# Kernel tuning notes

Measured on AMD Instinct MI355X. Metric: run time of the kernel, lower is better.

The kernel has to match this reference:

```python
import jax, jax.numpy as jnp
import numpy as np

B, V, H, L = 2, 256, 128, 3
GROUPS = 32  # GroupNorm32 in the 'normalization' head
EPS = 1e-5


def _layernorm(z, g, b):
    m = jnp.mean(z, -1, keepdims=True)
    v = jnp.var(z, -1, keepdims=True)
    return (z - m) * jax.lax.rsqrt(v + EPS) * g + b


def _forward(x, adj_matrix, emb_type, W_node, b_node, W_eattr, b_eattr, W_ee, b_ee,
             Wu, bu, Wv, bv, Wa, ba, Wb, bb, Wc, bc,
             lnh_g, lnh_b, lne_g, lne_b, plo_g, plo_b, plo_W, plo_bW,
             gn_g, gn_b, W_out, b_out):
    # node embed: Embedding(2,H) lookup -> Linear(H,H)
    h = emb_type[x] @ W_node + b_node                      # B V H
    ea = jnp.transpose(adj_matrix, (0, 2, 3, 1))           # B V V 6
    # edge embed: Linear(6,H) -> Linear(H,H)
    e = (ea @ W_eattr + b_eattr) @ W_ee + b_ee             # B V V H
    # graph = graph[..., -6].long(): binary adjacency channel, no grad
    mask = jax.lax.stop_gradient(ea[..., 0])               # B V V
    for l in range(L):
        h_in, e_in = h, e
        # gated anisotropic GCN layer (DIFUSCO GNNLayer, mode='direct')
        Uh = h @ Wu[l] + bu[l]                             # B V H
        Vh = h @ Wv[l] + bv[l]                             # B V H
        e_new = ((h @ Wa[l] + ba[l])[:, None, :, :]
                 + (h @ Wb[l] + bb[l])[:, :, None, :]
                 + (e @ Wc[l] + bc[l]))                    # B V V H
        gates = jax.nn.sigmoid(e_new) * mask[..., None]    # B V V H
        agg = jnp.einsum('bijh,bjh->bih', gates, Vh)       # gated 'sum' aggregation
        h = jax.nn.relu(_layernorm(Uh + agg, lnh_g[l], lnh_b[l]))
        e = jax.nn.relu(_layernorm(e_new, lne_g[l], lne_b[l]))
        # outer residual (GNNDi.dense_forward) + per_layer_out: LN -> SiLU -> Linear
        h = h_in + h
        e = e_in + (jax.nn.silu(_layernorm(e, plo_g[l], plo_b[l])) @ plo_W[l] + plo_bW[l])
    # head: GroupNorm(32,H) -> ReLU -> Conv2d(H, out_channels, 1) on B H V V
    z = jnp.transpose(e, (0, 3, 1, 2))                     # B H V V
    zg = z.reshape(B, GROUPS, H // GROUPS, V, V)
    mu = jnp.mean(zg, axis=(2, 3, 4), keepdims=True)
    var = jnp.var(zg, axis=(2, 3, 4), keepdims=True)
    z = ((zg - mu) * jax.lax.rsqrt(var + EPS)).reshape(B, H, V, V)
    z = jax.nn.relu(z * gn_g[None, :, None, None] + gn_b[None, :, None, None])
    return jnp.einsum('bchw,oc->bohw', z, W_out) + b_out[None, :, None, None]


def setup_inputs() -> dict:
    key = jax.random.key(0)
    ks = jax.random.split(key, 16)
    nrm = lambda k, s: jax.random.normal(k, s, dtype=jnp.float32) * 0.05
    adj = jnp.concatenate([
        (jax.random.uniform(ks[1], (B, 1, V, V)) < 0.15).astype(jnp.float32),  # channel 0: adjacency
        jax.random.normal(ks[2], (B, 5, V, V), dtype=jnp.float32)], axis=1)
    return {
        'x': jax.random.randint(ks[0], (B, V), 0, 2),
        'adj_matrix': adj,
        'emb_type': nrm(ks[3], (2, H)),
        'W_node': nrm(ks[4], (H, H)), 'b_node': jnp.zeros((H,), jnp.float32),
        'W_eattr': nrm(ks[5], (6, H)), 'b_eattr': jnp.zeros((H,), jnp.float32),
        'W_ee': nrm(ks[6], (H, H)), 'b_ee': jnp.zeros((H,), jnp.float32),
        'Wu': nrm(ks[7], (L, H, H)), 'bu': jnp.zeros((L, H), jnp.float32),
        'Wv': nrm(ks[8], (L, H, H)), 'bv': jnp.zeros((L, H), jnp.float32),
        'Wa': nrm(ks[9], (L, H, H)), 'ba': jnp.zeros((L, H), jnp.float32),
        'Wb': nrm(ks[10], (L, H, H)), 'bb': jnp.zeros((L, H), jnp.float32),
        'Wc': nrm(ks[11], (L, H, H)), 'bc': jnp.zeros((L, H), jnp.float32),
        'lnh_g': jnp.ones((L, H), jnp.float32), 'lnh_b': jnp.zeros((L, H), jnp.float32),
        'lne_g': jnp.ones((L, H), jnp.float32), 'lne_b': jnp.zeros((L, H), jnp.float32),
        'plo_g': jnp.ones((L, H), jnp.float32), 'plo_b': jnp.zeros((L, H), jnp.float32),
        'plo_W': nrm(ks[12], (L, H, H)), 'plo_bW': jnp.zeros((L, H), jnp.float32),
        'gn_g': jnp.ones((H,), jnp.float32), 'gn_b': jnp.zeros((H,), jnp.float32),
        'W_out': nrm(ks[13], (1, H)), 'b_out': jnp.zeros((1,), jnp.float32),
    }


def reference(x, adj_matrix, emb_type, W_node, b_node, W_eattr, b_eattr, W_ee, b_ee,
              Wu, bu, Wv, bv, Wa, ba, Wb, bb, Wc, bc,
              lnh_g, lnh_b, lne_g, lne_b, plo_g, plo_b, plo_W, plo_bW,
              gn_g, gn_b, W_out, b_out):
    return _forward(x, adj_matrix, emb_type, W_node, b_node, W_eattr, b_eattr, W_ee, b_ee,
                    Wu, bu, Wv, bv, Wa, ba, Wb, bb, Wc, bc,
                    lnh_g, lnh_b, lne_g, lne_b, plo_g, plo_b, plo_W, plo_bW,
                    gn_g, gn_b, W_out, b_out)
```

## Files before the change

### kernel.cpp

```cpp
#include <hip/hip_runtime.h>
#include <cstdint>
#include <cstddef>


#define EPSV 1e-5f

typedef __attribute__((ext_vector_type(8))) short short8v;
typedef __attribute__((ext_vector_type(4))) float f32x4;

__device__ __forceinline__ float sigmoidf_(float x) { return 1.f / (1.f + __expf(-x)); }

__device__ __forceinline__ unsigned short f2bf(float x) {
    unsigned int u = __float_as_uint(x);
    unsigned int r = u + 0x7FFFu + ((u >> 16) & 1u);
    return (unsigned short)(r >> 16);
}
__device__ __forceinline__ float bf2f(unsigned short u) {
    return __uint_as_float(((unsigned int)u) << 16);
}
__device__ __forceinline__ unsigned int cvtpk(float a, float b) {
    unsigned int r;
    asm("v_cvt_pk_bf16_f32 %0, %1, %2" : "=v"(r) : "v"(a), "v"(b));
    return r;
}
#define SWZ(row, cb) ((cb) ^ (((row) & 7) << 4))

__global__ void k_prep(const int* __restrict__ x, const float* __restrict__ emb,
                       const float* __restrict__ W_node, const float* __restrict__ b_node,
                       float* __restrict__ h, float* __restrict__ aggB,
                       const float* __restrict__ W_ea, const float* __restrict__ b_ea,
                       const float* __restrict__ W_ee, const float* __restrict__ b_ee,
                       float* __restrict__ Wcb, float* __restrict__ bcb,
                       const float* __restrict__ Wc, const float* __restrict__ PW,
                       unsigned short* __restrict__ WT)
{
    const int blk = blockIdx.x, t = threadIdx.x;
    if (blk < 512) {
        __shared__ float se[128];
        if (t < 128) { se[t] = emb[x[blk]*128 + t]; aggB[blk*128 + t] = 0.f; }
        __syncthreads();
        if (t < 128) {
            float acc = b_node[t];
            for (int k = 0; k < 128; ++k) acc = fmaf(se[k], W_node[k*128+t], acc);
            h[blk*128+t] = acc;
        }
    } else if (blk == 512) {
        if (t < 128) {
            float wc0=0,wc1=0,wc2=0,wc3=0,wc4=0,wc5=0,bv=0;
            for (int m = 0; m < 128; ++m) {
                float we = W_ee[m*128 + t];
                wc0 = fmaf(W_ea[0*128+m], we, wc0);
                wc1 = fmaf(W_ea[1*128+m], we, wc1);
                wc2 = fmaf(W_ea[2*128+m], we, wc2);
                wc3 = fmaf(W_ea[3*128+m], we, wc3);
                wc4 = fmaf(W_ea[4*128+m], we, wc4);
                wc5 = fmaf(W_ea[5*128+m], we, wc5);
                bv  = fmaf(b_ea[m], we, bv);
            }
            Wcb[0*128+t]=wc0; Wcb[1*128+t]=wc1; Wcb[2*128+t]=wc2;
            Wcb[3*128+t]=wc3; Wcb[4*128+t]=wc4; Wcb[5*128+t]=wc5;
            bcb[t] = bv + b_ee[t];
        }
    } else {
        const int m = blk - 513;
        const int l = m >> 1;
        const float* src = (m & 1) ? (PW + (size_t)l*16384) : (Wc + (size_t)l*16384);
        unsigned short* dst = WT + (size_t)m*16384;
        for (int idx = t; idx < 16384; idx += 256) {
            int n = idx >> 7, k = idx & 127;
            dst[idx] = f2bf(src[k*128 + n]);
        }
    }
}

__global__ void k_hgemm(float* __restrict__ h, float* __restrict__ Uh, float* __restrict__ aggB,
    const float* __restrict__ Wu_l, const float* __restrict__ bu_l,
    const float* __restrict__ Wv_l, const float* __restrict__ bv_l,
    const float* __restrict__ Wa_l, const float* __restrict__ ba_l,
    const float* __restrict__ Wb_l, const float* __restrict__ bb_l,
    float* __restrict__ VhT, float* __restrict__ AhT, float* __restrict__ Bh,
    const float* __restrict__ lnh_g, const float* __restrict__ lnh_b, int upd)
{
    __shared__ float sh[128];
    __shared__ float sred[4];
    int blk = blockIdx.x, t = threadIdx.x;
    int b = blk >> 8, v = blk & 255;
    float hv_ = h[blk*128 + t];
    if (upd) {
        float val = Uh[blk*128 + t] + aggB[blk*128 + t];
        aggB[blk*128 + t] = 0.f;
        float s = val, q = val*val;
        #pragma unroll
        for (int off = 32; off; off >>= 1) { s += __shfl_down(s, off); q += __shfl_down(q, off); }
        if ((t & 63) == 0) { sred[t>>6] = s; sred[2 + (t>>6)] = q; }
        __syncthreads();
        s = sred[0] + sred[1]; q = sred[2] + sred[3];
        float mean = s * (1.f/128.f);
        float var  = q * (1.f/128.f) - mean*mean;
        float nv = (val - mean) * rsqrtf(var + EPSV) * lnh_g[t] + lnh_b[t];
        hv_ += fmaxf(nv, 0.f);
        h[blk*128 + t] = hv_;
    }
    sh[t] = hv_;
    __syncthreads();
    float au=bu_l[t], av=bv_l[t], aa=ba_l[t], ab=bb_l[t];
    for (int k = 0; k < 128; ++k) {
        float hv = sh[k];
        au = fmaf(hv, Wu_l[k*128+t], au);
        av = fmaf(hv, Wv_l[k*128+t], av);
        aa = fmaf(hv, Wa_l[k*128+t], aa);
        ab = fmaf(hv, Wb_l[k*128+t], ab);
    }
    Uh[blk*128+t]=au; Bh[blk*128+t]=ab;
    VhT[(size_t)(b*128+t)*256 + v] = av;
    AhT[(size_t)(b*128+t)*256 + v] = aa;
}

template<int EINIT, int DO_AGG, int DO_STATS>
__global__ __launch_bounds__(256) void k_layer(
    unsigned short* __restrict__ e,
    const unsigned short* __restrict__ WcT, const unsigned short* __restrict__ PWT,
    const float* __restrict__ bc_l,
    const float* __restrict__ AhT, const float* __restrict__ Bh,
    const float* __restrict__ VhT, const float* __restrict__ adj,
    const float* __restrict__ lne_g, const float* __restrict__ lne_b,
    const float* __restrict__ plo_g, const float* __restrict__ plo_b,
    const float* __restrict__ pbW_l,
    float* __restrict__ aggB,
    const float* __restrict__ Wcb, const float* __restrict__ bcb,
    float* __restrict__ ggsum, float* __restrict__ ggsq)
{
    __shared__ __align__(16) char sW[32768];
    __shared__ float sRedA[512];
    __shared__ float sRedB[512];

    const int t = threadIdx.x;
    const int bi = blockIdx.x >> 2, chunk = blockIdx.x & 3;
    const int b = bi >> 8, i = bi & 255;
    const int w = t >> 6, lane = t & 63;
    const int lane16 = lane & 15, g = lane >> 4;
    const size_t rowbase = (size_t)bi * 32768;
    const int j0 = chunk*64 + w*16;
    char* sE = sW + w*4096;

    short8v a8[4];
    float am[6];
    if (EINIT) {
        const float* adjp = adj + (size_t)b*393216 + (size_t)i*256 + (j0 + lane16);
        #pragma unroll
        for (int m = 0; m < 6; ++m) am[m] = adjp[(size_t)m*65536];
        #pragma unroll
        for (int kst = 0; kst < 4; ++kst) {
            short8v v;
            #pragma unroll
            for (int e2 = 0; e2 < 4; ++e2) {
                const int h0 = kst*32 + g*8 + e2*2;
                float v0 = bcb[h0], v1 = bcb[h0+1];
                #pragma unroll
                for (int m = 0; m < 6; ++m) {
                    v0 = fmaf(am[m], Wcb[m*128 + h0],     v0);
                    v1 = fmaf(am[m], Wcb[m*128 + h0 + 1], v1);
                }
                const unsigned int p = cvtpk(v0, v1);
                v[e2*2]   = (short)(unsigned short)p;
                v[e2*2+1] = (short)(unsigned short)(p >> 16);
            }
            a8[kst] = v;
        }
    } else {
        const unsigned short* arow = e + rowbase + (size_t)(j0 + lane16)*128 + g*8;
        #pragma unroll
        for (int kst = 0; kst < 4; ++kst)
            a8[kst] = *(const short8v*)&arow[kst*32];
    }

    #pragma unroll
    for (int p = 0; p < 8; ++p) {
        const int idx = t*8 + p*2048;
        const int n = idx >> 7, cb = (idx & 127) << 1;
        *(short8v*)(sW + n*256 + SWZ(n, cb)) = *(const short8v*)&WcT[idx];
    }
    __syncthreads();

    f32x4 tv[8];
    float agg[8];
    float s1[4] = {0,0,0,0}, q1[4] = {0,0,0,0};
    const int jb = j0 + g*4;
    float4 mk;
    if (DO_AGG) mk = *(const float4*)&adj[(size_t)b*393216 + (size_t)i*256 + jb];
    const float* mkp = (const float*)&mk;
    #pragma unroll
    for (int nt = 0; nt < 8; ++nt) {
        const int col = nt*16 + lane16;
        f32x4 acc = {0.f,0.f,0.f,0.f};
        #pragma unroll
        for (int kst = 0; kst < 4; ++kst) {
            short8v bfr = *(const short8v*)(sW + col*256 + SWZ(col, kst*64 + g*16));
            acc = __builtin_amdgcn_mfma_f32_16x16x32_bf16(a8[kst], bfr, acc, 0, 0, 0);
        }
        const float bcB = bc_l[col] + Bh[bi*128 + col];
        const float4 ah = *(const float4*)&AhT[(size_t)(b*128+col)*256 + jb];
        const float* ahp = (const float*)&ah;
        if (DO_AGG) {
            const float4 vh = *(const float4*)&VhT[(size_t)(b*128+col)*256 + jb];
            const float* vhp = (const float*)&vh;
            float a = 0.f;
            #pragma unroll
            for (int r = 0; r < 4; ++r) {
                float tvl = acc[r] + bcB + ahp[r];
                a = fmaf(mkp[r]*sigmoidf_(tvl), vhp[r], a);
                s1[r] += tvl; q1[r] = fmaf(tvl, tvl, q1[r]);
                tv[nt][r] = tvl;
            }
            agg[nt] = a;
        } else {
            #pragma unroll
            for (int r = 0; r < 4; ++r) {
                float tvl = acc[r] + bcB + ahp[r];
                s1[r] += tvl; q1[r] = fmaf(tvl, tvl, q1[r]);
                tv[nt][r] = tvl;
            }
        }
    }
    float mu1[4], rs1[4];
    #pragma unroll
    for (int r = 0; r < 4; ++r) {
        float s = s1[r], q = q1[r];
        s += __shfl_xor(s,1); q += __shfl_xor(q,1);
        s += __shfl_xor(s,2); q += __shfl_xor(q,2);
        s += __shfl_xor(s,4); q += __shfl_xor(q,4);
        s += __shfl_xor(s,8); q += __shfl_xor(q,8);
        float mu = s*(1.f/128.f);
        mu1[r] = mu; rs1[r] = rsqrtf(q*(1.f/128.f) - mu*mu + EPSV);
    }
    float s2[4] = {0,0,0,0}, q2[4] = {0,0,0,0};
    #pragma unroll
    for (int nt = 0; nt < 8; ++nt) {
        const int col = nt*16 + lane16;
        const float lg = lne_g[col], lb = lne_b[col];
        #pragma unroll
        for (int r = 0; r < 4; ++r) {
            float tp = fmaxf(fmaf((tv[nt][r]-mu1[r])*rs1[r], lg, lb), 0.f);
            tv[nt][r] = tp;
            s2[r] += tp; q2[r] = fmaf(tp, tp, q2[r]);
        }
    }
    float mu2[4], rs2[4];
    #pragma unroll
    for (int r = 0; r < 4; ++r) {
        float s = s2[r], q = q2[r];
        s += __shfl_xor(s,1); q += __shfl_xor(q,1);
        s += __shfl_xor(s,2); q += __shfl_xor(q,2);
        s += __shfl_xor(s,4); q += __shfl_xor(q,4);
        s += __shfl_xor(s,8); q += __shfl_xor(q,8);
        float mu = s*(1.f/128.f);
        mu2[r] = mu; rs2[r] = rsqrtf(q*(1.f/128.f) - mu*mu + EPSV);
    }

    __syncthreads();

    #pragma unroll
    for (int nt = 0; nt < 8; ++nt) {
        const int col = nt*16 + lane16;
        const float pg = plo_g[col], pb = plo_b[col];
        float u[4];
        #pragma unroll
        for (int r = 0; r < 4; ++r) {
            float uu = fmaf((tv[nt][r]-mu2[r])*rs2[r], pg, pb);
            u[r] = uu * sigmoidf_(uu);
        }
        const unsigned int p01 = cvtpk(u[0], u[1]);
        const unsigned int p23 = cvtpk(u[2], u[3]);
        const int r0 = g*4;
        *(unsigned short*)(sE + (r0+0)*256 + SWZ(r0+0, col*2)) = (unsigned short)p01;
        *(unsigned short*)(sE + (r0+1)*256 + SWZ(r0+1, col*2)) = (unsigned short)(p01 >> 16);
        *(unsigned short*)(sE + (r0+2)*256 + SWZ(r0+2, col*2)) = (unsigned short)p23;
        *(unsigned short*)(sE + (r0+3)*256 + SWZ(r0+3, col*2)) = (unsigned short)(p23 >> 16);
    }
    short8v b8[4];
    #pragma unroll
    for (int kst = 0; kst < 4; ++kst)
        b8[kst] = *(const short8v*)(sE + lane16*256 + SWZ(lane16, kst*64 + g*16));

    __syncthreads();
    #pragma unroll
    for (int p = 0; p < 8; ++p) {
        const int idx = t*8 + p*2048;
        const int n = idx >> 7, cb = (idx & 127) << 1;
        *(short8v*)(sW + n*256 + SWZ(n, cb)) = *(const short8v*)&PWT[idx];
    }
    __syncthreads();

    const int jg = j0 + lane16;
    float gs[8], gq[8];
    #pragma unroll
    for (int nt = 0; nt < 8; ++nt) {
        const int an = nt*16 + lane16;
        f32x4 acc = {0.f,0.f,0.f,0.f};
        #pragma unroll
        for (int kst = 0; kst < 4; ++kst) {
            short8v aw = *(const short8v*)(sW + an*256 + SWZ(an, kst*64 + g*16));
            acc = __builtin_amdgcn_mfma_f32_16x16x32_bf16(aw, b8[kst], acc, 0, 0, 0);
        }
        const int n0 = nt*16 + g*4;
        const float4 pw4 = *(const float4*)&pbW_l[n0];
        const float* pwp = (const float*)&pw4;
        unsigned short* ep = &e[rowbase + (size_t)jg*128 + n0];
        float res[4];
        if (EINIT) {
            #pragma unroll
            for (int r = 0; r < 4; ++r) {
                float v0 = bcb[n0 + r];
                #pragma unroll
                for (int m = 0; m < 6; ++m) v0 = fmaf(am[m], Wcb[m*128 + n0 + r], v0);
                res[r] = v0;
            }
        } else {
            const ushort4 ev = *(const ushort4*)ep;
            res[0] = bf2f(ev.x); res[1] = bf2f(ev.y); res[2] = bf2f(ev.z); res[3] = bf2f(ev.w);
        }
        const float o0 = acc[0] + (pwp[0] + res[0]);
        const float o1 = acc[1] + (pwp[1] + res[1]);
        const float o2 = acc[2] + (pwp[2] + res[2]);
        const float o3 = acc[3] + (pwp[3] + res[3]);
        if (DO_STATS) {
            gs[nt] = (o0 + o1) + (o2 + o3);
            gq[nt] = fmaf(o0,o0, fmaf(o1,o1, fmaf(o2,o2, o3*o3)));
        }
        uint2 st;
        st.x = cvtpk(o0, o1);
        st.y = cvtpk(o2, o3);
        *(uint2*)ep = st;
    }

    if (DO_AGG) {
        #pragma unroll
        for (int nt = 0; nt < 8; ++nt) {
            float a = agg[nt];
            a += __shfl_xor(a, 16); a += __shfl_xor(a, 32);
            if (lane < 16) sRedA[w*128 + nt*16 + lane] = a;
        }
        __syncthreads();
        if (t < 128) {
            float S = sRedA[t] + sRedA[128+t] + sRedA[256+t] + sRedA[384+t];
            atomicAdd(&aggB[bi*128 + t], S);
        }
    }
    if (DO_STATS) {
        #pragma unroll
        for (int nt = 0; nt < 8; ++nt) {
            float a = gs[nt], qq = gq[nt];
            a += __shfl_xor(a, 1); qq += __shfl_xor(qq, 1);
            a += __shfl_xor(a, 2); qq += __shfl_xor(qq, 2);
            a += __shfl_xor(a, 4); qq += __shfl_xor(qq, 4);
            a += __shfl_xor(a, 8); qq += __shfl_xor(qq, 8);
            if (lane16 == 0) {
                sRedA[w*32 + nt*4 + g] = a;
                sRedB[w*32 + nt*4 + g] = qq;
            }
        }
        __syncthreads();
        if (t < 32) {
            float S = sRedA[t] + sRedA[32+t] + sRedA[64+t] + sRedA[96+t];
            float Q = sRedB[t] + sRedB[32+t] + sRedB[64+t] + sRedB[96+t];
            atomicAdd(&ggsum[b*32 + t], S);
            atomicAdd(&ggsq[b*32 + t], Q);
        }
    }
}

__global__ void k_gfin(const float* __restrict__ ggsum, const float* __restrict__ ggsq,
                       float* __restrict__ gmu, float* __restrict__ grs)
{
    int t = threadIdx.x;
    float s = ggsum[t], q = ggsq[t];
    const float invN = 1.f/(4.f*65536.f);
    float mu = s*invN;
    float var = q*invN - mu*mu;
    gmu[t] = mu;
    grs[t] = rsqrtf(var + EPSV);
}

__global__ __launch_bounds__(256) void k_head(
    const unsigned short* __restrict__ e, const float* __restrict__ gmu,
    const float* __restrict__ grs, const float* __restrict__ gn_g,
    const float* __restrict__ gn_b, const float* __restrict__ W_out,
    const float* __restrict__ b_out, float* __restrict__ out)
{
    const int blk = blockIdx.x, t = threadIdx.x;
    const int b = blk >> 8;
    const int ch8 = (t & 15)*8, jgrp = t >> 4;
    float gg[8], gb[8], wo[8];
    #pragma unroll
    for (int c = 0; c < 8; ++c) {
        const int ch = ch8 + c;
        const float mu = gmu[b*32 + (ch>>2)], rs = grs[b*32 + (ch>>2)];
        gg[c] = gn_g[ch]*rs;
        gb[c] = gn_b[ch] - mu*gg[c];
        wo[c] = W_out[ch];
    }
    const float bo = b_out[0];
    const unsigned short* erow = e + (size_t)blk*32768;
    float* orow = out + (size_t)blk*256;
    for (int it = 0; it < 16; ++it) {
        const int j = jgrp*16 + it;
        short8v v = *(const short8v*)&erow[(size_t)j*128 + ch8];
        float p = 0.f;
        #pragma unroll
        for (int c = 0; c < 8; ++c) {
            float f = bf2f((unsigned short)v[c]);
            p = fmaf(fmaxf(fmaf(f, gg[c], gb[c]), 0.f), wo[c], p);
        }
        p += __shfl_xor(p, 1); p += __shfl_xor(p, 2);
        p += __shfl_xor(p, 4); p += __shfl_xor(p, 8);
        if ((t & 15) == 0) orow[j] = p + bo;
    }
}

extern "C" void kernel_launch(void* const* d_in, const int* in_sizes, int n_in,
                              void* d_out, int out_size, void* d_ws, size_t ws_size,
                              hipStream_t stream)
{
    const int*   x      = (const int*)  d_in[0];
    const float* adj    = (const float*)d_in[1];
    const float* emb    = (const float*)d_in[2];
    const float* W_node = (const float*)d_in[3];
    const float* b_node = (const float*)d_in[4];
    const float* W_ea   = (const float*)d_in[5];
    const float* b_ea   = (const float*)d_in[6];
    const float* W_ee   = (const float*)d_in[7];
    const float* b_ee   = (const float*)d_in[8];
    const float* Wu     = (const float*)d_in[9];
    const float* bu     = (const float*)d_in[10];
    const float* Wv     = (const float*)d_in[11];
    const float* bv     = (const float*)d_in[12];
    const float* Wa     = (const float*)d_in[13];
    const float* ba     = (const float*)d_in[14];
    const float* Wb     = (const float*)d_in[15];
    const float* bb     = (const float*)d_in[16];
    const float* Wc     = (const float*)d_in[17];
    const float* bc     = (const float*)d_in[18];
    const float* lnh_g  = (const float*)d_in[19];
    const float* lnh_b  = (const float*)d_in[20];
    const float* lne_g  = (const float*)d_in[21];
    const float* lne_b  = (const float*)d_in[22];
    const float* plo_g  = (const float*)d_in[23];
    const float* plo_b  = (const float*)d_in[24];
    const float* plo_W  = (const float*)d_in[25];
    const float* plo_bW = (const float*)d_in[26];
    const float* gn_g   = (const float*)d_in[27];
    const float* gn_b   = (const float*)d_in[28];
    const float* W_out  = (const float*)d_in[29];
    const float* b_out  = (const float*)d_in[30];
    float* out = (float*)d_out;

    float* ws = (float*)d_ws;
    size_t off = 0;
    unsigned short* e = (unsigned short*)(ws + off); off += 8388608;
    float* h    = ws + off; off += 65536;
    float* Uh   = ws + off; off += 65536;
    float* Bh   = ws + off; off += 65536;
    float* VhT  = ws + off; off += 65536;
    float* AhT  = ws + off; off += 65536;
    float* aggB = ws + off; off += 65536;
    float* Wcb  = ws + off; off += 768;
    float* bcb  = ws + off; off += 128;
    float* ggsum = ws + off; off += 64;
    float* ggsq  = ws + off; off += 64;
    float* gmu  = ws + off; off += 64;
    float* grs  = ws + off; off += 64;
    unsigned short* WT = (unsigned short*)(ws + off); off += 49152;

    k_prep<<<519, 256, 0, stream>>>(x, emb, W_node, b_node, h, aggB,
                                    W_ea, b_ea, W_ee, b_ee, Wcb, bcb,
                                    Wc, plo_W, WT);
    hipMemsetAsync(ggsum, 0, 512, stream);

    for (int l = 0; l < 3; ++l) {
        k_hgemm<<<512, 128, 0, stream>>>(h, Uh, aggB,
            Wu + (size_t)l*16384, bu + l*128,
            Wv + (size_t)l*16384, bv + l*128,
            Wa + (size_t)l*16384, ba + l*128,
            Wb + (size_t)l*16384, bb + l*128,
            VhT, AhT, Bh,
            lnh_g + (l==0?0:(l-1)*128), lnh_b + (l==0?0:(l-1)*128), l > 0 ? 1 : 0);
        const unsigned short* WcT_l = WT + (size_t)(2*l)*16384;
        const unsigned short* PWT_l = WT + (size_t)(2*l+1)*16384;
        if (l == 0) {
            k_layer<1,1,0><<<2048, 256, 0, stream>>>(e, WcT_l, PWT_l,
                bc + l*128, AhT, Bh, VhT, adj,
                lne_g + l*128, lne_b + l*128,
                plo_g + l*128, plo_b + l*128,
                plo_bW + l*128, aggB, Wcb, bcb, ggsum, ggsq);
        } else if (l == 1) {
            k_layer<0,1,0><<<2048, 256, 0, stream>>>(e, WcT_l, PWT_l,
                bc + l*128, AhT, Bh, VhT, adj,
                lne_g + l*128, lne_b + l*128,
                plo_g + l*128, plo_b + l*128,
                plo_bW + l*128, aggB, Wcb, bcb, ggsum, ggsq);
        } else {
            k_layer<0,0,1><<<2048, 256, 0, stream>>>(e, WcT_l, PWT_l,
                bc + l*128, AhT, Bh, VhT, adj,
                lne_g + l*128, lne_b + l*128,
                plo_g + l*128, plo_b + l*128,
                plo_bW + l*128, aggB, Wcb, bcb, ggsum, ggsq);
        }
    }

    k_gfin<<<1, 64, 0, stream>>>(ggsum, ggsq, gmu, grs);
    k_head<<<512, 256, 0, stream>>>(e, gmu, grs, gn_g, gn_b, W_out, b_out, out);
}
```

Before: 234.5 us.

## Double-buffer Wc and plo_W in LDS, use 512-thread blocks per half-row

The per-layer edge kernel now uses 512-thread blocks, each covering half of an edge row instead of a quarter. Both weight matrices (Wc and the per-layer-out weight) are loaded into separate LDS buffers up front, which removes the mid-kernel barrier pair and the weight reload between the two GEMMs. The first layer now writes the initial edge embedding to global memory during init and reads it back as the residual, instead of recomputing it from the adjacency. This halves weight staging per edge, at the cost of more LDS per block (about 69 KB) and so fewer resident blocks.

New measurement: 250.3 us. 6.7% more time.

```diff
diff --git a/kernel.cpp b/kernel.cpp
--- a/kernel.cpp
+++ b/kernel.cpp
@@ -117,7 +117,7 @@
 }
 
 template<int EINIT, int DO_AGG, int DO_STATS>
-__global__ __launch_bounds__(256) void k_layer(
+__global__ __launch_bounds__(512, 4) void k_layer(
     unsigned short* __restrict__ e,
     const unsigned short* __restrict__ WcT, const unsigned short* __restrict__ PWT,
     const float* __restrict__ bc_l,
@@ -130,42 +130,51 @@
     const float* __restrict__ Wcb, const float* __restrict__ bcb,
     float* __restrict__ ggsum, float* __restrict__ ggsq)
 {
-    __shared__ __align__(16) char sW[32768];
-    __shared__ float sRedA[512];
-    __shared__ float sRedB[512];
+    __shared__ __align__(16) char sW1[32768];
+    __shared__ __align__(16) char sW2[32768];
+    __shared__ float sRedA[1024];
+    __shared__ float sRedB[256];
 
     const int t = threadIdx.x;
-    const int bi = blockIdx.x >> 2, chunk = blockIdx.x & 3;
+    const int bi = blockIdx.x >> 1, half = blockIdx.x & 1;
     const int b = bi >> 8, i = bi & 255;
     const int w = t >> 6, lane = t & 63;
     const int lane16 = lane & 15, g = lane >> 4;
     const size_t rowbase = (size_t)bi * 32768;
-    const int j0 = chunk*64 + w*16;
-    char* sE = sW + w*4096;
+    const int j0 = half*128 + w*16;
+    char* sE = sW1 + w*4096;
 
     short8v a8[4];
-    float am[6];
     if (EINIT) {
+        float am[6];
         const float* adjp = adj + (size_t)b*393216 + (size_t)i*256 + (j0 + lane16);
         #pragma unroll
         for (int m = 0; m < 6; ++m) am[m] = adjp[(size_t)m*65536];
+        unsigned short* erow = &e[rowbase + (size_t)(j0 + lane16)*128];
         #pragma unroll
         for (int kst = 0; kst < 4; ++kst) {
-            short8v v;
+            const int base = kst*32 + g*8;
+            float4 v0 = *(const float4*)&bcb[base];
+            float4 v1 = *(const float4*)&bcb[base+4];
+            float vv[8] = {v0.x, v0.y, v0.z, v0.w, v1.x, v1.y, v1.z, v1.w};
             #pragma unroll
-            for (int e2 = 0; e2 < 4; ++e2) {
-                const int h0 = kst*32 + g*8 + e2*2;
-                float v0 = bcb[h0], v1 = bcb[h0+1];
-                #pragma unroll
-                for (int m = 0; m < 6; ++m) {
-                    v0 = fmaf(am[m], Wcb[m*128 + h0],     v0);
-                    v1 = fmaf(am[m], Wcb[m*128 + h0 + 1], v1);
-                }
-                const unsigned int p = cvtpk(v0, v1);
-                v[e2*2]   = (short)(unsigned short)p;
-                v[e2*2+1] = (short)(unsigned short)(p >> 16);
+            for (int m = 0; m < 6; ++m) {
+                const float4 w0 = *(const float4*)&Wcb[m*128 + base];
+                const float4 w1 = *(const float4*)&Wcb[m*128 + base + 4];
+                vv[0] = fmaf(am[m], w0.x, vv[0]); vv[1] = fmaf(am[m], w0.y, vv[1]);
+                vv[2] = fmaf(am[m], w0.z, vv[2]); vv[3] = fmaf(am[m], w0.w, vv[3]);
+                vv[4] = fmaf(am[m], w1.x, vv[4]); vv[5] = fmaf(am[m], w1.y, vv[5]);
+                vv[6] = fmaf(am[m], w1.z, vv[6]); vv[7] = fmaf(am[m], w1.w, vv[7]);
             }
-            a8[kst] = v;
+            short8v vfr;
+            #pragma unroll
+            for (int pr = 0; pr < 4; ++pr) {
+                const unsigned int p = cvtpk(vv[pr*2], vv[pr*2+1]);
+                vfr[pr*2]   = (short)(unsigned short)p;
+                vfr[pr*2+1] = (short)(unsigned short)(p >> 16);
+            }
+            a8[kst] = vfr;
+            *(short8v*)&erow[base] = vfr;
         }
     } else {
         const unsigned short* arow = e + rowbase + (size_t)(j0 + lane16)*128 + g*8;
@@ -175,10 +184,11 @@
     }
 
     #pragma unroll
-    for (int p = 0; p < 8; ++p) {
-        const int idx = t*8 + p*2048;
+    for (int p = 0; p < 4; ++p) {
+        const int idx = t*8 + p*4096;
         const int n = idx >> 7, cb = (idx & 127) << 1;
-        *(short8v*)(sW + n*256 + SWZ(n, cb)) = *(const short8v*)&WcT[idx];
+        *(short8v*)(sW1 + n*256 + SWZ(n, cb)) = *(const short8v*)&WcT[idx];
+        *(short8v*)(sW2 + n*256 + SWZ(n, cb)) = *(const short8v*)&PWT[idx];
     }
     __syncthreads();
 
@@ -195,7 +205,7 @@
         f32x4 acc = {0.f,0.f,0.f,0.f};
         #pragma unroll
         for (int kst = 0; kst < 4; ++kst) {
-            short8v bfr = *(const short8v*)(sW + col*256 + SWZ(col, kst*64 + g*16));
+            short8v bfr = *(const short8v*)(sW1 + col*256 + SWZ(col, kst*64 + g*16));
             acc = __builtin_amdgcn_mfma_f32_16x16x32_bf16(a8[kst], bfr, acc, 0, 0, 0);
         }
         const float bcB = bc_l[col] + Bh[bi*128 + col];
@@ -282,15 +292,6 @@
     for (int kst = 0; kst < 4; ++kst)
         b8[kst] = *(const short8v*)(sE + lane16*256 + SWZ(lane16, kst*64 + g*16));
 
-    __syncthreads();
-    #pragma unroll
-    for (int p = 0; p < 8; ++p) {
-        const int idx = t*8 + p*2048;
-        const int n = idx >> 7, cb = (idx & 127) << 1;
-        *(short8v*)(sW + n*256 + SWZ(n, cb)) = *(const short8v*)&PWT[idx];
-    }
-    __syncthreads();
-
     const int jg = j0 + lane16;
     float gs[8], gq[8];
     #pragma unroll
@@ -299,30 +300,18 @@
         f32x4 acc = {0.f,0.f,0.f,0.f};
         #pragma unroll
         for (int kst = 0; kst < 4; ++kst) {
-            short8v aw = *(const short8v*)(sW + an*256 + SWZ(an, kst*64 + g*16));
+            short8v aw = *(const short8v*)(sW2 + an*256 + SWZ(an, kst*64 + g*16));
             acc = __builtin_amdgcn_mfma_f32_16x16x32_bf16(aw, b8[kst], acc, 0, 0, 0);
         }
         const int n0 = nt*16 + g*4;
         const float4 pw4 = *(const float4*)&pbW_l[n0];
         const float* pwp = (const float*)&pw4;
         unsigned short* ep = &e[rowbase + (size_t)jg*128 + n0];
-        float res[4];
-        if (EINIT) {
-            #pragma unroll
-            for (int r = 0; r < 4; ++r) {
-                float v0 = bcb[n0 + r];
-                #pragma unroll
-                for (int m = 0; m < 6; ++m) v0 = fmaf(am[m], Wcb[m*128 + n0 + r], v0);
-                res[r] = v0;
-            }
-        } else {
-            const ushort4 ev = *(const ushort4*)ep;
-            res[0] = bf2f(ev.x); res[1] = bf2f(ev.y); res[2] = bf2f(ev.z); res[3] = bf2f(ev.w);
-        }
-        const float o0 = acc[0] + (pwp[0] + res[0]);
-        const float o1 = acc[1] + (pwp[1] + res[1]);
-        const float o2 = acc[2] + (pwp[2] + res[2]);
-        const float o3 = acc[3] + (pwp[3] + res[3]);
+        const ushort4 ev = *(const ushort4*)ep;
+        const float o0 = acc[0] + (pwp[0] + bf2f(ev.x));
+        const float o1 = acc[1] + (pwp[1] + bf2f(ev.y));
+        const float o2 = acc[2] + (pwp[2] + bf2f(ev.z));
+        const float o3 = acc[3] + (pwp[3] + bf2f(ev.w));
         if (DO_STATS) {
             gs[nt] = (o0 + o1) + (o2 + o3);
             gq[nt] = fmaf(o0,o0, fmaf(o1,o1, fmaf(o2,o2, o3*o3)));
@@ -342,7 +331,9 @@
         }
         __syncthreads();
         if (t < 128) {
-            float S = sRedA[t] + sRedA[128+t] + sRedA[256+t] + sRedA[384+t];
+            float S = 0.f;
+            #pragma unroll
+            for (int k = 0; k < 8; ++k) S += sRedA[k*128 + t];
             atomicAdd(&aggB[bi*128 + t], S);
         }
     }
@@ -361,8 +352,9 @@
         }
         __syncthreads();
         if (t < 32) {
-            float S = sRedA[t] + sRedA[32+t] + sRedA[64+t] + sRedA[96+t];
-            float Q = sRedB[t] + sRedB[32+t] + sRedB[64+t] + sRedB[96+t];
+            float S = 0.f, Q = 0.f;
+            #pragma unroll
+            for (int k = 0; k < 8; ++k) { S += sRedA[k*32 + t]; Q += sRedB[k*32 + t]; }
             atomicAdd(&ggsum[b*32 + t], S);
             atomicAdd(&ggsq[b*32 + t], Q);
         }
@@ -487,19 +479,19 @@
         const unsigned short* WcT_l = WT + (size_t)(2*l)*16384;
         const unsigned short* PWT_l = WT + (size_t)(2*l+1)*16384;
         if (l == 0) {
-            k_layer<1,1,0><<<2048, 256, 0, stream>>>(e, WcT_l, PWT_l,
+            k_layer<1,1,0><<<1024, 512, 0, stream>>>(e, WcT_l, PWT_l,
                 bc + l*128, AhT, Bh, VhT, adj,
                 lne_g + l*128, lne_b + l*128,
                 plo_g + l*128, plo_b + l*128,
                 plo_bW + l*128, aggB, Wcb, bcb, ggsum, ggsq);
         } else if (l == 1) {
-            k_layer<0,1,0><<<2048, 256, 0, stream>>>(e, WcT_l, PWT_l,
+            k_layer<0,1,0><<<1024, 512, 0, stream>>>(e, WcT_l, PWT_l,
                 bc + l*128, AhT, Bh, VhT, adj,
                 lne_g + l*128, lne_b + l*128,
                 plo_g + l*128, plo_b + l*128,
                 plo_bW + l*128, aggB, Wcb, bcb, ggsum, ggsq);
         } else {
-            k_layer<0,0,1><<<2048, 256, 0, stream>>>(e, WcT_l, PWT_l,
+            k_layer<0,0,1><<<1024, 512, 0, stream>>>(e, WcT_l, PWT_l,
                 bc + l*128, AhT, Bh, VhT, adj,
                 lne_g + l*128, lne_b + l*128,
                 plo_g + l*128, plo_b + l*128,
```
